# Performance work log

Measured on AMD Instinct MI355X. Metric: run time of the kernel, lower is better.

Reference implementation:

```python
import jax, jax.numpy as jnp
import numpy as np

GROUPS = 8
EPS = 1e-5


def group_norm_dim1(x, gamma, beta):
    # Faithful to torch: GroupNorm treats dim 1 (height) as the channel axis.
    B, H, W, C = x.shape
    xg = x.reshape(B, GROUPS, H // GROUPS, W, C)
    mean = xg.mean(axis=(2, 3, 4), keepdims=True)
    var = xg.var(axis=(2, 3, 4), keepdims=True)
    xn = ((xg - mean) * jax.lax.rsqrt(var + EPS)).reshape(B, H, W, C)
    return xn * gamma[None, :, None, None] + beta[None, :, None, None]


def setup_inputs() -> dict:
    key = jax.random.key(0)
    ks = jax.random.split(key, 8)
    B, H, W, C = 4, 64, 64, 64  # height must equal units for GroupNorm to apply
    s = 1.0 / np.sqrt(C)
    return {
        "x": jax.random.normal(ks[0], (B, H, W, C), dtype=jnp.float32),
        "gamma": jnp.ones((C,), jnp.float32),
        "beta": jnp.zeros((C,), jnp.float32),
        "Wq": jax.random.normal(ks[1], (C, C), jnp.float32) * s,
        "bq": jnp.zeros((C,), jnp.float32),
        "Wk": jax.random.normal(ks[2], (C, C), jnp.float32) * s,
        "bk": jnp.zeros((C,), jnp.float32),
        "Wv": jax.random.normal(ks[3], (C, C), jnp.float32) * s,
        "bv": jnp.zeros((C,), jnp.float32),
        "Wo": jax.random.normal(ks[4], (C, C), jnp.float32) * s,
        "bo": jnp.zeros((C,), jnp.float32),
    }


def reference(x, gamma, beta, Wq, bq, Wk, bk, Wv, bv, Wo, bo):
    B, H, W, C = x.shape
    scale = C ** (-0.5)
    xn = group_norm_dim1(x, gamma, beta)
    q = xn @ Wq + bq
    k = xn @ Wk + bk
    v = xn @ Wv + bv
    # full spatial self-attention: scores [B, H, W, H*W]
    scores = jnp.einsum('bhwc,bijc->bhwij', q, k) * scale
    attn = jax.nn.softmax(scores.reshape(B, H, W, H * W), axis=-1)
    attn = attn.reshape(B, H, W, H, W)
    proj = jnp.einsum('bhwij,bijc->bhwc', attn, v)
    proj = proj @ Wo + bo
    return xn + proj
```

## Files before the change

### kernel.cpp

```cpp
#include <hip/hip_runtime.h>

typedef __bf16 bf16_t;
typedef bf16_t bf16x8 __attribute__((ext_vector_type(8)));
typedef bf16_t bf16x4 __attribute__((ext_vector_type(4)));
typedef short  short4v __attribute__((ext_vector_type(4)));
typedef float  f32x4  __attribute__((ext_vector_type(4)));

#define MFMA32(a, b, c) __builtin_amdgcn_mfma_f32_16x16x32_bf16(a, b, c, 0, 0, 0)
#define MFMA16(a, b, c) __builtin_amdgcn_mfma_f32_16x16x16bf16_1k(a, b, c, 0, 0, 0)

__global__ __launch_bounds__(256) void gn1w_kernel(const float* __restrict__ x,
    float2* __restrict__ partials,
    const float* __restrict__ Wq, const float* __restrict__ Wk,
    const float* __restrict__ Wv, const float* __restrict__ Wo,
    bf16_t* __restrict__ Wt) {
  int blk = blockIdx.x, t = threadIdx.x;
  if (blk >= 256) {
    int idx = (blk - 256) * 256 + t;
    int wsel = idx >> 12, rem = idx & 4095;
    int c = rem >> 6, kk = rem & 63;
    const float* src = (wsel == 0) ? Wq : ((wsel == 1) ? Wk : ((wsel == 2) ? Wv : Wo));
    Wt[idx] = (bf16_t)src[kk * 64 + c];
    return;
  }
  const float4* x4 = (const float4*)x + (size_t)blk * 1024;
  float s = 0.f, sq = 0.f;
  #pragma unroll
  for (int u = 0; u < 4; ++u) {
    float4 v = x4[u * 256 + t];
    s  += v.x + v.y + v.z + v.w;
    sq += v.x * v.x + v.y * v.y + v.z * v.z + v.w * v.w;
  }
  for (int off = 32; off; off >>= 1) {
    s  += __shfl_down(s, off, 64);
    sq += __shfl_down(sq, off, 64);
  }
  __shared__ float2 ps[4];
  if ((t & 63) == 0) ps[t >> 6] = make_float2(s, sq);
  __syncthreads();
  if (t == 0) {
    float S = 0.f, Q = 0.f;
    #pragma unroll
    for (int i = 0; i < 4; ++i) { S += ps[i].x; Q += ps[i].y; }
    partials[blk] = make_float2(S, Q);
  }
}

__global__ __launch_bounds__(256) void gnqkv_kernel(
    const float* __restrict__ x, const float* __restrict__ gamma,
    const float* __restrict__ beta, const float2* __restrict__ parts,
    const bf16_t* __restrict__ Wt,
    const float* __restrict__ bq, const float* __restrict__ bk, const float* __restrict__ bv,
    bf16_t* __restrict__ xnb, bf16_t* __restrict__ qo, bf16_t* __restrict__ ko,
    bf16_t* __restrict__ vo) {
  __shared__ __align__(16) bf16_t xl[4096];
  int blk = blockIdx.x, t = threadIdx.x;
  int grp = blk >> 3;
  float S = 0.f, Q = 0.f;
  #pragma unroll
  for (int i = 0; i < 8; ++i) { float2 p = parts[grp * 8 + i]; S += p.x; Q += p.y; }
  float mean = S * (1.f / 32768.f);
  float rstd = rsqrtf(Q * (1.f / 32768.f) - mean * mean + 1e-5f);
  int h = blk & 63;
  float ga = gamma[h] * rstd;
  float be = beta[h] - mean * ga;
  {
    int r = t >> 2, col0 = (t & 3) * 16;
    const float4* x4 = (const float4*)(x + (size_t)blk * 4096 + r * 64 + col0);
    bf16x8 pk0, pk1;
    float4 v0 = x4[0], v1 = x4[1], v2 = x4[2], v3 = x4[3];
    pk0[0] = (bf16_t)(v0.x * ga + be); pk0[1] = (bf16_t)(v0.y * ga + be);
    pk0[2] = (bf16_t)(v0.z * ga + be); pk0[3] = (bf16_t)(v0.w * ga + be);
    pk0[4] = (bf16_t)(v1.x * ga + be); pk0[5] = (bf16_t)(v1.y * ga + be);
    pk0[6] = (bf16_t)(v1.z * ga + be); pk0[7] = (bf16_t)(v1.w * ga + be);
    pk1[0] = (bf16_t)(v2.x * ga + be); pk1[1] = (bf16_t)(v2.y * ga + be);
    pk1[2] = (bf16_t)(v2.z * ga + be); pk1[3] = (bf16_t)(v2.w * ga + be);
    pk1[4] = (bf16_t)(v3.x * ga + be); pk1[5] = (bf16_t)(v3.y * ga + be);
    pk1[6] = (bf16_t)(v3.z * ga + be); pk1[7] = (bf16_t)(v3.w * ga + be);
    *(bf16x8*)&xnb[(size_t)blk * 4096 + r * 64 + col0]     = pk0;
    *(bf16x8*)&xnb[(size_t)blk * 4096 + r * 64 + col0 + 8] = pk1;
    int sw = r & 7, j0 = (t & 3) * 2;
    *(bf16x8*)&xl[r * 64 + ((j0 ^ sw) << 3)]       = pk0;
    *(bf16x8*)&xl[r * 64 + (((j0 + 1) ^ sw) << 3)] = pk1;
  }
  __syncthreads();
  int w = t >> 6, lane = t & 63, quad = lane >> 4, l16 = lane & 15;
  int rl = w * 16 + l16, sw2 = rl & 7;
  bf16x8 a0 = *(const bf16x8*)&xl[rl * 64 + ((quad ^ sw2) << 3)];
  bf16x8 a1 = *(const bf16x8*)&xl[rl * 64 + (((quad + 4) ^ sw2) << 3)];
  int m0 = blk * 64 + w * 16;
  int bi = m0 >> 12, kk0 = (m0 & 4095) + quad * 4;
  f32x4 zero = {0.f, 0.f, 0.f, 0.f};
  const float QSCALE = 0.125f * 1.44269504088896340736f;
  #pragma unroll
  for (int outk = 0; outk < 3; ++outk) {
    const bf16_t* wt = Wt + outk * 4096;
    const float* bias = (outk == 0) ? bq : ((outk == 1) ? bk : bv);
    #pragma unroll
    for (int nt = 0; nt < 4; ++nt) {
      int col = nt * 16 + l16;
      bf16x8 b0 = *(const bf16x8*)&wt[col * 64 + quad * 8];
      bf16x8 b1 = *(const bf16x8*)&wt[col * 64 + 32 + quad * 8];
      f32x4 acc = MFMA32(a0, b0, zero);
      acc = MFMA32(a1, b1, acc);
      float bb = bias[col];
      if (outk == 2) {
        bf16x4 pk;
        #pragma unroll
        for (int r = 0; r < 4; ++r) pk[r] = (bf16_t)(acc[r] + bb);
        *(bf16x4*)&vo[(size_t)bi * 262144 + (size_t)(kk0 >> 2) * 256 + col * 4] = pk;
      } else {
        #pragma unroll
        for (int r = 0; r < 4; ++r) {
          int m = m0 + quad * 4 + r;
          float v = acc[r] + bb;
          if (outk == 0) qo[(size_t)m * 64 + col] = (bf16_t)(v * QSCALE);
          else           ko[(size_t)m * 64 + col] = (bf16_t)v;
        }
      }
    }
  }
}

__global__ __launch_bounds__(256, 4) void flash_kernel(
    const bf16_t* __restrict__ q, const bf16_t* __restrict__ k,
    const bf16_t* __restrict__ vp, bf16_t* __restrict__ Opb, float* __restrict__ ml) {
  __shared__ float redO[2][2048];
  __shared__ float redL[2][128];
  int t = threadIdx.x;
  int w = t >> 6, lane = t & 63, quad = lane >> 4, l16 = lane & 15;
  int g = w >> 1, kw = w & 1;
  int b = blockIdx.y, sp = blockIdx.z;
  int q0 = blockIdx.x * 64 + g * 32;

  bf16x8 qf[2][2];
  {
    const bf16_t* qp = q + ((size_t)b * 4096 + q0 + l16) * 64;
    #pragma unroll
    for (int qt = 0; qt < 2; ++qt)
      #pragma unroll
      for (int hh = 0; hh < 2; ++hh)
        qf[qt][hh] = *(const bf16x8*)&qp[qt * 1024 + hh * 32 + quad * 8];
  }
  f32x4 o[2][4];
  f32x4 zero = {0.f, 0.f, 0.f, 0.f};
  #pragma unroll
  for (int qt = 0; qt < 2; ++qt)
    #pragma unroll
    for (int ct = 0; ct < 4; ++ct) o[qt][ct] = zero;
  float rs[2] = {0.f, 0.f};

  const bf16_t* kbase = k  + (size_t)b * 262144;
  const bf16_t* vbase = vp + (size_t)b * 262144;
  int key00 = sp * 1024 + kw * 512;

  for (int step = 0; step < 16; ++step) {
    int key0 = key00 + step * 32;
    bf16x8 ka[2][2];
    #pragma unroll
    for (int kt = 0; kt < 2; ++kt)
      #pragma unroll
      for (int hh = 0; hh < 2; ++hh)
        ka[kt][hh] = *(const bf16x8*)&kbase[(size_t)(key0 + kt * 16 + l16) * 64 + hh * 32 + quad * 8];
    short4v va[4][2];
    #pragma unroll
    for (int kt = 0; kt < 2; ++kt) {
      int cb = ((key0 + kt * 16) >> 2) + quad;
      #pragma unroll
      for (int ct = 0; ct < 4; ++ct)
        va[ct][kt] = *(const short4v*)&vbase[(size_t)cb * 256 + (ct * 16 + l16) * 4];
    }
    #pragma unroll
    for (int kt = 0; kt < 2; ++kt) {
      #pragma unroll
      for (int qt = 0; qt < 2; ++qt) {
        f32x4 st = MFMA32(ka[kt][0], qf[qt][0], zero);
        st = MFMA32(ka[kt][1], qf[qt][1], st);
        bf16x4 pb;
        float psum = 0.f;
        #pragma unroll
        for (int r = 0; r < 4; ++r) {
          float p = __builtin_amdgcn_exp2f(st[r]);
          psum += p;
          pb[r] = (bf16_t)p;
        }
        rs[qt] += psum;
        short4v pshort = __builtin_bit_cast(short4v, pb);
        #pragma unroll
        for (int ct = 0; ct < 4; ++ct)
          o[qt][ct] = MFMA16(va[ct][kt], pshort, o[qt][ct]);
      }
    }
  }
  #pragma unroll
  for (int qt = 0; qt < 2; ++qt) {
    rs[qt] += __shfl_xor(rs[qt], 16, 64);
    rs[qt] += __shfl_xor(rs[qt], 32, 64);
  }
  if (kw == 1) {
    #pragma unroll
    for (int qt = 0; qt < 2; ++qt) {
      #pragma unroll
      for (int ct = 0; ct < 4; ++ct)
        #pragma unroll
        for (int r = 0; r < 4; ++r)
          redO[g][((qt * 4 + ct) * 4 + r) * 64 + lane] = o[qt][ct][r];
      redL[g][qt * 64 + lane] = rs[qt];
    }
  }
  __syncthreads();
  if (kw == 0) {
    int slot = sp * 4 + b;
    #pragma unroll
    for (int qt = 0; qt < 2; ++qt) {
      float lt = rs[qt] + redL[g][qt * 64 + lane];
      if (quad == 0) ml[(size_t)slot * 4096 + q0 + qt * 16 + l16] = lt;
      #pragma unroll
      for (int ct = 0; ct < 4; ++ct) {
        bf16x4 pk;
        #pragma unroll
        for (int r = 0; r < 4; ++r)
          pk[r] = (bf16_t)(o[qt][ct][r] + redO[g][((qt * 4 + ct) * 4 + r) * 64 + lane]);
        *(bf16x4*)&Opb[((size_t)slot * 4096 + q0 + qt * 16 + l16) * 64 + ct * 16 + quad * 4] = pk;
      }
    }
  }
}

__global__ __launch_bounds__(256) void proj_kernel(
    const bf16_t* __restrict__ Opb, const float* __restrict__ ml,
    const bf16_t* __restrict__ Wt, const float* __restrict__ bo,
    const bf16_t* __restrict__ xnb, float* __restrict__ out) {
  int t = threadIdx.x, w = t >> 6, lane = t & 63, quad = lane >> 4, l16 = lane & 15;
  int blk = blockIdx.x;
  int b = blk >> 6;
  int rowb = ((blk & 63) * 64) + w * 16;
  float acc0[8], acc1[8];
  #pragma unroll
  for (int e = 0; e < 8; ++e) { acc0[e] = 0.f; acc1[e] = 0.f; }
  float lsum = 0.f;
  #pragma unroll
  for (int s = 0; s < 4; ++s) {
    size_t rr = (size_t)(s * 4 + b) * 4096 + rowb + l16;
    bf16x8 f0 = *(const bf16x8*)&Opb[rr * 64 + quad * 8];
    bf16x8 f1 = *(const bf16x8*)&Opb[rr * 64 + 32 + quad * 8];
    #pragma unroll
    for (int e = 0; e < 8; ++e) { acc0[e] += (float)f0[e]; acc1[e] += (float)f1[e]; }
    lsum += ml[rr];
  }
  float linv = 1.f / lsum;
  bf16x8 a0, a1;
  #pragma unroll
  for (int e = 0; e < 8; ++e) {
    a0[e] = (bf16_t)(acc0[e] * linv);
    a1[e] = (bf16_t)(acc1[e] * linv);
  }
  f32x4 zero = {0.f, 0.f, 0.f, 0.f};
  const bf16_t* wt = Wt + 3 * 4096;
  int m0 = blk * 64 + w * 16;
  #pragma unroll
  for (int nt = 0; nt < 4; ++nt) {
    int col = nt * 16 + l16;
    bf16x8 b0 = *(const bf16x8*)&wt[col * 64 + quad * 8];
    bf16x8 b1 = *(const bf16x8*)&wt[col * 64 + 32 + quad * 8];
    f32x4 acc = MFMA32(a0, b0, zero);
    acc = MFMA32(a1, b1, acc);
    float bb = bo[col];
    #pragma unroll
    for (int r = 0; r < 4; ++r) {
      size_t m = (size_t)m0 + quad * 4 + r;
      out[m * 64 + col] = acc[r] + bb + (float)xnb[m * 64 + col];
    }
  }
}

extern "C" void kernel_launch(void* const* d_in, const int* in_sizes, int n_in,
                              void* d_out, int out_size, void* d_ws, size_t ws_size,
                              hipStream_t stream) {
  const float* x     = (const float*)d_in[0];
  const float* gamma = (const float*)d_in[1];
  const float* beta  = (const float*)d_in[2];
  const float* Wq    = (const float*)d_in[3];
  const float* bq    = (const float*)d_in[4];
  const float* Wk    = (const float*)d_in[5];
  const float* bk    = (const float*)d_in[6];
  const float* Wv    = (const float*)d_in[7];
  const float* bv    = (const float*)d_in[8];
  const float* Wo    = (const float*)d_in[9];
  const float* bo    = (const float*)d_in[10];
  float* out = (float*)d_out;

  char* ws = (char*)d_ws;
  bf16_t* xnb   = (bf16_t*)(ws + 0);
  bf16_t* qb    = (bf16_t*)(ws + (2u  << 20));
  bf16_t* kb    = (bf16_t*)(ws + (4u  << 20));
  bf16_t* vb    = (bf16_t*)(ws + (6u  << 20));
  bf16_t* Opb   = (bf16_t*)(ws + (8u  << 20));
  float*  ml    = (float*)(ws + (16u << 20));
  float2* parts = (float2*)(ws + (17u << 20));
  bf16_t* Wt    = (bf16_t*)(ws + (17u << 20) + 4096);

  hipLaunchKernelGGL(gn1w_kernel,  dim3(320),      dim3(256), 0, stream, x, parts, Wq, Wk, Wv, Wo, Wt);
  hipLaunchKernelGGL(gnqkv_kernel, dim3(256),      dim3(256), 0, stream, x, gamma, beta, parts, Wt, bq, bk, bv, xnb, qb, kb, vb);
  hipLaunchKernelGGL(flash_kernel, dim3(64, 4, 4), dim3(256), 0, stream, qb, kb, vb, Opb, ml);
  hipLaunchKernelGGL(proj_kernel,  dim3(256),      dim3(256), 0, stream, Opb, ml, Wt, bo, xnb, out);
}
```

Before: 143.0 us.

## Split flash keys across four waves per query tile and prefetch K fragments

Each flash block now handles 32 queries instead of 64, with all four waves splitting the block's 1024-key range into 256-key chunks. The grid doubles along x to keep coverage, and a two-stage tree reduction through shared memory combines the four partial O and row sums. K fragments are double-buffered in registers so the next step's loads are issued before the current MFMAs, and the launch-bounds occupancy hint rises to 5. The aim is more parallelism and hidden load latency, at the cost of more Q loads per key, extra syncs and LDS traffic, and register pressure.

```diff
diff --git a/kernel.cpp b/kernel.cpp
--- a/kernel.cpp
+++ b/kernel.cpp
@@ -122,16 +122,15 @@
   }
 }
 
-__global__ __launch_bounds__(256, 4) void flash_kernel(
+__global__ __launch_bounds__(256, 5) void flash_kernel(
     const bf16_t* __restrict__ q, const bf16_t* __restrict__ k,
     const bf16_t* __restrict__ vp, bf16_t* __restrict__ Opb, float* __restrict__ ml) {
   __shared__ float redO[2][2048];
   __shared__ float redL[2][128];
   int t = threadIdx.x;
   int w = t >> 6, lane = t & 63, quad = lane >> 4, l16 = lane & 15;
-  int g = w >> 1, kw = w & 1;
   int b = blockIdx.y, sp = blockIdx.z;
-  int q0 = blockIdx.x * 64 + g * 32;
+  int q0 = blockIdx.x * 32;
 
   bf16x8 qf[2][2];
   {
@@ -152,16 +151,19 @@
 
   const bf16_t* kbase = k  + (size_t)b * 262144;
   const bf16_t* vbase = vp + (size_t)b * 262144;
-  int key00 = sp * 1024 + kw * 512;
-
-  for (int step = 0; step < 16; ++step) {
+  int key00 = sp * 1024 + w * 256;
+
+  bf16x8 kf[2][2][2];
+  #pragma unroll
+  for (int kt = 0; kt < 2; ++kt)
+    #pragma unroll
+    for (int hh = 0; hh < 2; ++hh)
+      kf[0][kt][hh] = *(const bf16x8*)&kbase[(size_t)(key00 + kt * 16 + l16) * 64 + hh * 32 + quad * 8];
+
+  #pragma unroll
+  for (int step = 0; step < 8; ++step) {
+    int cur = step & 1;
     int key0 = key00 + step * 32;
-    bf16x8 ka[2][2];
-    #pragma unroll
-    for (int kt = 0; kt < 2; ++kt)
-      #pragma unroll
-      for (int hh = 0; hh < 2; ++hh)
-        ka[kt][hh] = *(const bf16x8*)&kbase[(size_t)(key0 + kt * 16 + l16) * 64 + hh * 32 + quad * 8];
     short4v va[4][2];
     #pragma unroll
     for (int kt = 0; kt < 2; ++kt) {
@@ -170,12 +172,20 @@
       for (int ct = 0; ct < 4; ++ct)
         va[ct][kt] = *(const short4v*)&vbase[(size_t)cb * 256 + (ct * 16 + l16) * 4];
     }
+    if (step < 7) {
+      int kn0 = key0 + 32;
+      #pragma unroll
+      for (int kt = 0; kt < 2; ++kt)
+        #pragma unroll
+        for (int hh = 0; hh < 2; ++hh)
+          kf[cur ^ 1][kt][hh] = *(const bf16x8*)&kbase[(size_t)(kn0 + kt * 16 + l16) * 64 + hh * 32 + quad * 8];
+    }
     #pragma unroll
     for (int kt = 0; kt < 2; ++kt) {
       #pragma unroll
       for (int qt = 0; qt < 2; ++qt) {
-        f32x4 st = MFMA32(ka[kt][0], qf[qt][0], zero);
-        st = MFMA32(ka[kt][1], qf[qt][1], st);
+        f32x4 st = MFMA32(kf[cur][kt][0], qf[qt][0], zero);
+        st = MFMA32(kf[cur][kt][1], qf[qt][1], st);
         bf16x4 pb;
         float psum = 0.f;
         #pragma unroll
@@ -197,30 +207,55 @@
     rs[qt] += __shfl_xor(rs[qt], 16, 64);
     rs[qt] += __shfl_xor(rs[qt], 32, 64);
   }
-  if (kw == 1) {
+  if (w >= 2) {
+    int buf = w - 2;
     #pragma unroll
     for (int qt = 0; qt < 2; ++qt) {
       #pragma unroll
       for (int ct = 0; ct < 4; ++ct)
         #pragma unroll
         for (int r = 0; r < 4; ++r)
-          redO[g][((qt * 4 + ct) * 4 + r) * 64 + lane] = o[qt][ct][r];
-      redL[g][qt * 64 + lane] = rs[qt];
-    }
-  }
-  __syncthreads();
-  if (kw == 0) {
+          redO[buf][((qt * 4 + ct) * 4 + r) * 64 + lane] = o[qt][ct][r];
+      redL[buf][qt * 64 + lane] = rs[qt];
+    }
+  }
+  __syncthreads();
+  if (w < 2) {
+    #pragma unroll
+    for (int qt = 0; qt < 2; ++qt) {
+      #pragma unroll
+      for (int ct = 0; ct < 4; ++ct)
+        #pragma unroll
+        for (int r = 0; r < 4; ++r)
+          o[qt][ct][r] += redO[w][((qt * 4 + ct) * 4 + r) * 64 + lane];
+      rs[qt] += redL[w][qt * 64 + lane];
+    }
+  }
+  __syncthreads();
+  if (w == 1) {
+    #pragma unroll
+    for (int qt = 0; qt < 2; ++qt) {
+      #pragma unroll
+      for (int ct = 0; ct < 4; ++ct)
+        #pragma unroll
+        for (int r = 0; r < 4; ++r)
+          redO[0][((qt * 4 + ct) * 4 + r) * 64 + lane] = o[qt][ct][r];
+      redL[0][qt * 64 + lane] = rs[qt];
+    }
+  }
+  __syncthreads();
+  if (w == 0) {
     int slot = sp * 4 + b;
     #pragma unroll
     for (int qt = 0; qt < 2; ++qt) {
-      float lt = rs[qt] + redL[g][qt * 64 + lane];
+      float lt = rs[qt] + redL[0][qt * 64 + lane];
       if (quad == 0) ml[(size_t)slot * 4096 + q0 + qt * 16 + l16] = lt;
       #pragma unroll
       for (int ct = 0; ct < 4; ++ct) {
         bf16x4 pk;
         #pragma unroll
         for (int r = 0; r < 4; ++r)
-          pk[r] = (bf16_t)(o[qt][ct][r] + redO[g][((qt * 4 + ct) * 4 + r) * 64 + lane]);
+          pk[r] = (bf16_t)(o[qt][ct][r] + redO[0][((qt * 4 + ct) * 4 + r) * 64 + lane]);
         *(bf16x4*)&Opb[((size_t)slot * 4096 + q0 + qt * 16 + l16) * 64 + ct * 16 + quad * 4] = pk;
       }
     }
@@ -300,8 +335,8 @@
   float2* parts = (float2*)(ws + (17u << 20));
   bf16_t* Wt    = (bf16_t*)(ws + (17u << 20) + 4096);
 
-  hipLaunchKernelGGL(gn1w_kernel,  dim3(320),      dim3(256), 0, stream, x, parts, Wq, Wk, Wv, Wo, Wt);
-  hipLaunchKernelGGL(gnqkv_kernel, dim3(256),      dim3(256), 0, stream, x, gamma, beta, parts, Wt, bq, bk, bv, xnb, qb, kb, vb);
-  hipLaunchKernelGGL(flash_kernel, dim3(64, 4, 4), dim3(256), 0, stream, qb, kb, vb, Opb, ml);
-  hipLaunchKernelGGL(proj_kernel,  dim3(256),      dim3(256), 0, stream, Opb, ml, Wt, bo, xnb, out);
-}
+  hipLaunchKernelGGL(gn1w_kernel,  dim3(320),       dim3(256), 0, stream, x, parts, Wq, Wk, Wv, Wo, Wt);
+  hipLaunchKernelGGL(gnqkv_kernel, dim3(256),       dim3(256), 0, stream, x, gamma, beta, parts, Wt, bq, bk, bv, xnb, qb, kb, vb);
+  hipLaunchKernelGGL(flash_kernel, dim3(128, 4, 4), dim3(256), 0, stream, qb, kb, vb, Opb, ml);
+  hipLaunchKernelGGL(proj_kernel,  dim3(256),       dim3(256), 0, stream, Opb, ml, Wt, bo, xnb, out);
+}
```

New measurement: 222.0 us. +55.2%, slower.

## Stage K/V tiles in double-buffered LDS and halve key splits in flash attention

Applied to the files above, without the earlier changes.

The flash kernel now loads 64-key K and V tiles cooperatively into swizzled, double-buffered shared memory, prefetching the next tile while computing the current one. Before, each wave read K/V fragments straight from global memory. V is written in a new channel-major blocked layout to match the LDS reads. The block shrinks to two waves with no intra-block key split and no LDS reduction, and the grid splits keys two ways instead of four, so proj sums two partials. This cuts redundant global K/V traffic and partial-output writes, at the cost of fewer concurrent blocks and a barrier on every tile.

```diff
diff --git a/kernel.cpp b/kernel.cpp
--- a/kernel.cpp
+++ b/kernel.cpp
@@ -89,7 +89,7 @@
   bf16x8 a0 = *(const bf16x8*)&xl[rl * 64 + ((quad ^ sw2) << 3)];
   bf16x8 a1 = *(const bf16x8*)&xl[rl * 64 + (((quad + 4) ^ sw2) << 3)];
   int m0 = blk * 64 + w * 16;
-  int bi = m0 >> 12, kk0 = (m0 & 4095) + quad * 4;
+  int bi = m0 >> 12;
   f32x4 zero = {0.f, 0.f, 0.f, 0.f};
   const float QSCALE = 0.125f * 1.44269504088896340736f;
   #pragma unroll
@@ -108,7 +108,8 @@
         bf16x4 pk;
         #pragma unroll
         for (int r = 0; r < 4; ++r) pk[r] = (bf16_t)(acc[r] + bb);
-        *(bf16x4*)&vo[(size_t)bi * 262144 + (size_t)(kk0 >> 2) * 256 + col * 4] = pk;
+        *(bf16x4*)&vo[(size_t)bi * 262144 + (size_t)(blk & 63) * 4096
+                      + (size_t)col * 64 + w * 16 + quad * 4] = pk;
       } else {
         #pragma unroll
         for (int r = 0; r < 4; ++r) {
@@ -122,16 +123,15 @@
   }
 }
 
-__global__ __launch_bounds__(256, 4) void flash_kernel(
+__global__ __launch_bounds__(128) void flash_kernel(
     const bf16_t* __restrict__ q, const bf16_t* __restrict__ k,
     const bf16_t* __restrict__ vp, bf16_t* __restrict__ Opb, float* __restrict__ ml) {
-  __shared__ float redO[2][2048];
-  __shared__ float redL[2][128];
+  __shared__ __align__(16) bf16_t Kb[2][4096];
+  __shared__ __align__(16) bf16_t Vb[2][4096];
   int t = threadIdx.x;
   int w = t >> 6, lane = t & 63, quad = lane >> 4, l16 = lane & 15;
-  int g = w >> 1, kw = w & 1;
-  int b = blockIdx.y, sp = blockIdx.z;
-  int q0 = blockIdx.x * 64 + g * 32;
+  int qb = blockIdx.x, b = blockIdx.y, sp = blockIdx.z;
+  int q0 = qb * 64 + w * 32;
 
   bf16x8 qf[2][2];
   {
@@ -150,32 +150,58 @@
     for (int ct = 0; ct < 4; ++ct) o[qt][ct] = zero;
   float rs[2] = {0.f, 0.f};
 
-  const bf16_t* kbase = k  + (size_t)b * 262144;
-  const bf16_t* vbase = vp + (size_t)b * 262144;
-  int key00 = sp * 1024 + kw * 512;
-
-  for (int step = 0; step < 16; ++step) {
-    int key0 = key00 + step * 32;
-    bf16x8 ka[2][2];
-    #pragma unroll
-    for (int kt = 0; kt < 2; ++kt)
-      #pragma unroll
-      for (int hh = 0; hh < 2; ++hh)
-        ka[kt][hh] = *(const bf16x8*)&kbase[(size_t)(key0 + kt * 16 + l16) * 64 + hh * 32 + quad * 8];
-    short4v va[4][2];
-    #pragma unroll
-    for (int kt = 0; kt < 2; ++kt) {
-      int cb = ((key0 + kt * 16) >> 2) + quad;
+  const bf16_t* kbase = k  + (size_t)b * 262144 + (size_t)sp * 131072;
+  const bf16_t* vbase = vp + (size_t)b * 262144 + (size_t)sp * 131072;
+
+  {
+    bf16x8 ks[4], vs[4];
+    #pragma unroll
+    for (int i = 0; i < 4; ++i) {
+      ks[i] = *(const bf16x8*)&kbase[i * 1024 + t * 8];
+      vs[i] = *(const bf16x8*)&vbase[i * 1024 + t * 8];
+    }
+    #pragma unroll
+    for (int i = 0; i < 4; ++i) {
+      int e = i * 1024 + t * 8;
+      int row = e >> 6;
+      int ch = (e >> 3) & 7;
+      *(bf16x8*)&Kb[0][row * 64 + ((ch ^ (row & 7)) << 3)] = ks[i];
+      int u = (e >> 2) & 15;
+      *(bf16x8*)&Vb[0][row * 64 + ((u ^ ((row & 7) << 1)) << 2)] = vs[i];
+    }
+  }
+  __syncthreads();
+
+  int swk = l16 & 7;
+  int swv = (l16 & 7) << 1;
+
+  for (int it = 0; it < 32; ++it) {
+    int cur = it & 1;
+    bf16x8 ks[4], vs[4];
+    if (it < 31) {
+      const bf16_t* kg = kbase + (it + 1) * 4096;
+      const bf16_t* vg = vbase + (it + 1) * 4096;
+      #pragma unroll
+      for (int i = 0; i < 4; ++i) {
+        ks[i] = *(const bf16x8*)&kg[i * 1024 + t * 8];
+        vs[i] = *(const bf16x8*)&vg[i * 1024 + t * 8];
+      }
+    }
+    const bf16_t* Kc = Kb[cur];
+    const bf16_t* Vc = Vb[cur];
+    #pragma unroll
+    for (int kt = 0; kt < 4; ++kt) {
+      int krow = (kt * 16 + l16) * 64;
+      bf16x8 kf0 = *(const bf16x8*)&Kc[krow + ((quad ^ swk) << 3)];
+      bf16x8 kf1 = *(const bf16x8*)&Kc[krow + (((quad + 4) ^ swk) << 3)];
+      short4v va[4];
       #pragma unroll
       for (int ct = 0; ct < 4; ++ct)
-        va[ct][kt] = *(const short4v*)&vbase[(size_t)cb * 256 + (ct * 16 + l16) * 4];
-    }
-    #pragma unroll
-    for (int kt = 0; kt < 2; ++kt) {
+        va[ct] = *(const short4v*)&Vc[(ct * 16 + l16) * 64 + (((kt * 4 + quad) ^ swv) << 2)];
       #pragma unroll
       for (int qt = 0; qt < 2; ++qt) {
-        f32x4 st = MFMA32(ka[kt][0], qf[qt][0], zero);
-        st = MFMA32(ka[kt][1], qf[qt][1], st);
+        f32x4 st = MFMA32(kf0, qf[qt][0], zero);
+        st = MFMA32(kf1, qf[qt][1], st);
         bf16x4 pb;
         float psum = 0.f;
         #pragma unroll
@@ -188,41 +214,40 @@
         short4v pshort = __builtin_bit_cast(short4v, pb);
         #pragma unroll
         for (int ct = 0; ct < 4; ++ct)
-          o[qt][ct] = MFMA16(va[ct][kt], pshort, o[qt][ct]);
+          o[qt][ct] = MFMA16(va[ct], pshort, o[qt][ct]);
       }
     }
-  }
+    if (it < 31) {
+      int nxt = cur ^ 1;
+      #pragma unroll
+      for (int i = 0; i < 4; ++i) {
+        int e = i * 1024 + t * 8;
+        int row = e >> 6;
+        int ch = (e >> 3) & 7;
+        *(bf16x8*)&Kb[nxt][row * 64 + ((ch ^ (row & 7)) << 3)] = ks[i];
+        int u = (e >> 2) & 15;
+        *(bf16x8*)&Vb[nxt][row * 64 + ((u ^ ((row & 7) << 1)) << 2)] = vs[i];
+      }
+    }
+    __syncthreads();
+  }
+
   #pragma unroll
   for (int qt = 0; qt < 2; ++qt) {
     rs[qt] += __shfl_xor(rs[qt], 16, 64);
     rs[qt] += __shfl_xor(rs[qt], 32, 64);
   }
-  if (kw == 1) {
-    #pragma unroll
-    for (int qt = 0; qt < 2; ++qt) {
-      #pragma unroll
-      for (int ct = 0; ct < 4; ++ct)
-        #pragma unroll
-        for (int r = 0; r < 4; ++r)
-          redO[g][((qt * 4 + ct) * 4 + r) * 64 + lane] = o[qt][ct][r];
-      redL[g][qt * 64 + lane] = rs[qt];
-    }
-  }
-  __syncthreads();
-  if (kw == 0) {
-    int slot = sp * 4 + b;
-    #pragma unroll
-    for (int qt = 0; qt < 2; ++qt) {
-      float lt = rs[qt] + redL[g][qt * 64 + lane];
-      if (quad == 0) ml[(size_t)slot * 4096 + q0 + qt * 16 + l16] = lt;
-      #pragma unroll
-      for (int ct = 0; ct < 4; ++ct) {
-        bf16x4 pk;
-        #pragma unroll
-        for (int r = 0; r < 4; ++r)
-          pk[r] = (bf16_t)(o[qt][ct][r] + redO[g][((qt * 4 + ct) * 4 + r) * 64 + lane]);
-        *(bf16x4*)&Opb[((size_t)slot * 4096 + q0 + qt * 16 + l16) * 64 + ct * 16 + quad * 4] = pk;
-      }
+  size_t rbase = (size_t)sp * 16384 + (size_t)b * 4096 + q0;
+  #pragma unroll
+  for (int qt = 0; qt < 2; ++qt) {
+    size_t row = rbase + qt * 16 + l16;
+    if (quad == 0) ml[row] = rs[qt];
+    #pragma unroll
+    for (int ct = 0; ct < 4; ++ct) {
+      bf16x4 pk;
+      #pragma unroll
+      for (int r = 0; r < 4; ++r) pk[r] = (bf16_t)o[qt][ct][r];
+      *(bf16x4*)&Opb[row * 64 + ct * 16 + quad * 4] = pk;
     }
   }
 }
@@ -232,16 +257,14 @@
     const bf16_t* __restrict__ Wt, const float* __restrict__ bo,
     const bf16_t* __restrict__ xnb, float* __restrict__ out) {
   int t = threadIdx.x, w = t >> 6, lane = t & 63, quad = lane >> 4, l16 = lane & 15;
-  int blk = blockIdx.x;
-  int b = blk >> 6;
-  int rowb = ((blk & 63) * 64) + w * 16;
+  int r0 = blockIdx.x * 64 + w * 16;
   float acc0[8], acc1[8];
   #pragma unroll
   for (int e = 0; e < 8; ++e) { acc0[e] = 0.f; acc1[e] = 0.f; }
   float lsum = 0.f;
   #pragma unroll
-  for (int s = 0; s < 4; ++s) {
-    size_t rr = (size_t)(s * 4 + b) * 4096 + rowb + l16;
+  for (int s = 0; s < 2; ++s) {
+    size_t rr = (size_t)s * 16384 + r0 + l16;
     bf16x8 f0 = *(const bf16x8*)&Opb[rr * 64 + quad * 8];
     bf16x8 f1 = *(const bf16x8*)&Opb[rr * 64 + 32 + quad * 8];
     #pragma unroll
@@ -257,7 +280,6 @@
   }
   f32x4 zero = {0.f, 0.f, 0.f, 0.f};
   const bf16_t* wt = Wt + 3 * 4096;
-  int m0 = blk * 64 + w * 16;
   #pragma unroll
   for (int nt = 0; nt < 4; ++nt) {
     int col = nt * 16 + l16;
@@ -268,7 +290,7 @@
     float bb = bo[col];
     #pragma unroll
     for (int r = 0; r < 4; ++r) {
-      size_t m = (size_t)m0 + quad * 4 + r;
+      size_t m = (size_t)r0 + quad * 4 + r;
       out[m * 64 + col] = acc[r] + bb + (float)xnb[m * 64 + col];
     }
   }
@@ -296,12 +318,12 @@
   bf16_t* kb    = (bf16_t*)(ws + (4u  << 20));
   bf16_t* vb    = (bf16_t*)(ws + (6u  << 20));
   bf16_t* Opb   = (bf16_t*)(ws + (8u  << 20));
-  float*  ml    = (float*)(ws + (16u << 20));
-  float2* parts = (float2*)(ws + (17u << 20));
-  bf16_t* Wt    = (bf16_t*)(ws + (17u << 20) + 4096);
-
-  hipLaunchKernelGGL(gn1w_kernel,  dim3(320),      dim3(256), 0, stream, x, parts, Wq, Wk, Wv, Wo, Wt);
-  hipLaunchKernelGGL(gnqkv_kernel, dim3(256),      dim3(256), 0, stream, x, gamma, beta, parts, Wt, bq, bk, bv, xnb, qb, kb, vb);
-  hipLaunchKernelGGL(flash_kernel, dim3(64, 4, 4), dim3(256), 0, stream, qb, kb, vb, Opb, ml);
-  hipLaunchKernelGGL(proj_kernel,  dim3(256),      dim3(256), 0, stream, Opb, ml, Wt, bo, xnb, out);
-}
+  float*  ml    = (float*)(ws + (12u << 20));
+  float2* parts = (float2*)(ws + (13u << 20));
+  bf16_t* Wt    = (bf16_t*)(ws + (13u << 20) + 4096);
+
+  hipLaunchKernelGGL(gn1w_kernel,  dim3(320),       dim3(256), 0, stream, x, parts, Wq, Wk, Wv, Wo, Wt);
+  hipLaunchKernelGGL(gnqkv_kernel, dim3(256),       dim3(256), 0, stream, x, gamma, beta, parts, Wt, bq, bk, bv, xnb, qb, kb, vb);
+  hipLaunchKernelGGL(flash_kernel, dim3(64, 4, 2),  dim3(128), 0, stream, qb, kb, vb, Opb, ml);
+  hipLaunchKernelGGL(proj_kernel,  dim3(256),       dim3(256), 0, stream, Opb, ml, Wt, bo, xnb, out);
+}
```

After: 138.9 us. 1.03x faster.
